# Kernel optimization log

Hardware: AMD Instinct MI355X
Metric: run time of the kernel (lower is better)

The kernel has to match this reference:

```python
import jax, jax.numpy as jnp
import numpy as np

N = 10000      # nodes
E = 160000     # edges
IN = 512       # in_feat
H = 512        # hidden_dim
L = 6          # layers
C = 64         # num_class
EPS = 1e-5     # BatchNorm eps


def setup_inputs() -> dict:
    key = jax.random.key(0)
    ks = jax.random.split(key, 12)
    x = jax.random.normal(ks[0], (N, IN), jnp.float32)
    src = jax.random.randint(ks[1], (E,), 0, N)
    dst = jax.random.randint(ks[2], (E,), 0, N)
    W0 = jax.random.normal(ks[3], (IN, H), jnp.float32) * (1.0 / np.sqrt(IN))
    Ws = jax.random.normal(ks[4], (L - 1, H, H), jnp.float32) * (1.0 / np.sqrt(H))
    bs = jnp.zeros((L, H), jnp.float32)
    gamma = jnp.ones((L, H), jnp.float32) + 0.1 * jax.random.normal(ks[5], (L, H), jnp.float32)
    beta = 0.1 * jax.random.normal(ks[6], (L, H), jnp.float32)
    run_mean = 0.1 * jax.random.normal(ks[7], (L, H), jnp.float32)
    run_var = jax.random.uniform(ks[8], (L, H), jnp.float32, 0.5, 1.5)
    linW = jax.random.normal(ks[9], (L * H, C), jnp.float32) * (1.0 / np.sqrt(L * H))
    linb = jnp.zeros((C,), jnp.float32)
    return {"x": x, "W0": W0, "Ws": Ws, "bs": bs, "gamma": gamma, "beta": beta,
            "run_mean": run_mean, "run_var": run_var, "linW": linW, "linb": linb,
            "src": src, "dst": dst}


def reference(x, W0, Ws, bs, gamma, beta, run_mean, run_var, linW, linb, src, dst):
    ones_e = jnp.ones((E,), jnp.float32)
    out_deg = jax.ops.segment_sum(ones_e, src, num_segments=N)
    in_deg = jax.ops.segment_sum(ones_e, dst, num_segments=N)
    # DGL GraphConv norm='both': D_dst^{-1/2} A D_src^{-1/2}, zero-deg clamped to 1
    norm_src = jnp.clip(out_deg, 1.0, None) ** -0.5   # [N]
    norm_dst = jnp.clip(in_deg, 1.0, None) ** -0.5    # [N]

    h = x
    hs = []
    for i in range(L):
        W = W0 if i == 0 else Ws[i - 1]
        m = (h * norm_src[:, None]) @ W                 # [N, H] GEMM
        agg = jax.ops.segment_sum(m[src], dst, num_segments=N)  # gather/scatter
        h = agg * norm_dst[:, None] + bs[i]
        # BatchNorm1d (inference, running stats) + ReLU; dropout is identity in eval
        scale = gamma[i] * jax.lax.rsqrt(run_var[i] + EPS)
        h = jax.nn.relu((h - run_mean[i]) * scale + beta[i])
        hs.append(h)
    h = jnp.concatenate(hs, axis=-1)                    # [N, L*H] JK-concat
    return h @ linW + linb                              # [N, C]
```

## Files before the change

### kernel.cpp

```cpp
#include <hip/hip_runtime.h>

#define NN 10000
#define NNPAD 10112
#define NE 160000
#define HF 512
#define LL 6
#define NC 64
#define KCAT (LL*HF)
#define BN_EPS 1e-5f
#define FSPLIT 3
#define AGG_SLOTS (((NN + 31) / 32) * 8)

typedef _Float16 f16x8 __attribute__((ext_vector_type(8)));
typedef _Float16 f16x4 __attribute__((ext_vector_type(4)));
typedef float f32x4 __attribute__((ext_vector_type(4)));

#define GLB(p) ((const __attribute__((address_space(1))) void*)(p))
#define LDSP(p) ((__attribute__((address_space(3))) void*)(p))

__global__ void deg_kernel(const int* __restrict__ src, const int* __restrict__ dst,
                           unsigned* __restrict__ cnt_out, unsigned* __restrict__ cnt_in) {
  int e = blockIdx.x * blockDim.x + threadIdx.x;
  if (e < NE) {
    atomicAdd(&cnt_out[src[e]], 1u);
    atomicAdd(&cnt_in[dst[e]], 1u);
  }
}

__global__ void fused_setup(const float* __restrict__ W0, const float* __restrict__ Ws,
                            const float* __restrict__ linW, const float* __restrict__ x,
                            const unsigned* __restrict__ cnt_out, const unsigned* __restrict__ cnt_in,
                            const float* __restrict__ bs, const float* __restrict__ gamma,
                            const float* __restrict__ beta, const float* __restrict__ rmean,
                            const float* __restrict__ rvar,
                            _Float16* __restrict__ Wt, _Float16* __restrict__ Lt,
                            _Float16* __restrict__ zh,
                            float* __restrict__ norm_src, float* __restrict__ norm_dst,
                            float* __restrict__ bnsc, float* __restrict__ bnsh) {
  __shared__ float t32[32][33];
  int b = blockIdx.x;
  int tid = threadIdx.x;
  if (b < 1536) {
    int l = b >> 8, r = b & 255;
    int n0 = (r & 15) * 32, k0 = (r >> 4) * 32;
    const float* W = (l == 0) ? W0 : (Ws + (size_t)(l - 1) * HF * HF);
    int tx = tid & 31, ty4 = (tid >> 5) * 4;
    #pragma unroll
    for (int j = 0; j < 4; ++j)
      t32[ty4 + j][tx] = W[(size_t)(k0 + ty4 + j) * HF + n0 + tx];
    __syncthreads();
    size_t base = (size_t)l * HF * HF;
    #pragma unroll
    for (int j = 0; j < 4; ++j)
      Wt[base + (size_t)(n0 + ty4 + j) * HF + k0 + tx] = (_Float16)t32[tx][ty4 + j];
  } else if (b < 1728) {
    int r = b - 1536;
    int n0 = (r & 1) * 32, k0 = (r >> 1) * 32;
    int tx = tid & 31, ty4 = (tid >> 5) * 4;
    #pragma unroll
    for (int j = 0; j < 4; ++j)
      t32[ty4 + j][tx] = linW[(size_t)(k0 + ty4 + j) * NC + n0 + tx];
    __syncthreads();
    #pragma unroll
    for (int j = 0; j < 4; ++j)
      Lt[(size_t)(n0 + ty4 + j) * KCAT + k0 + tx] = (_Float16)t32[tx][ty4 + j];
  } else if (b < 6728) {
    int i = (b - 1728) * 256 + tid;
    if (i < NN * HF / 4) {
      float4 v = *(const float4*)&x[i * 4];
      f16x4 h;
      h.x = (_Float16)v.x; h.y = (_Float16)v.y; h.z = (_Float16)v.z; h.w = (_Float16)v.w;
      *(f16x4*)&zh[i * 4] = h;
    }
  } else {
    int i = (b - 6728) * 256 + tid;
    if (i < NN) {
      unsigned co = cnt_out[i]; if (co < 1u) co = 1u;
      unsigned ci = cnt_in[i];  if (ci < 1u) ci = 1u;
      norm_src[i] = rsqrtf((float)co);
      norm_dst[i] = rsqrtf((float)ci);
    }
    if (i < LL * HF) {
      float s = gamma[i] * rsqrtf(rvar[i] + BN_EPS);
      bnsc[i] = s;
      bnsh[i] = (bs[i] - rmean[i]) * s + beta[i];
    }
  }
}

__global__ void scan_kernel(const unsigned* __restrict__ cnt, unsigned* __restrict__ off) {
  __shared__ unsigned wsum[4];
  const int T = 40;
  int tid = threadIdx.x;
  int lane = tid & 63, wv = tid >> 6;
  int start = tid * T;
  unsigned s = 0;
  for (int j = 0; j < T; ++j) {
    int i = start + j;
    if (i < NN) s += cnt[i];
  }
  unsigned x = s;
  #pragma unroll
  for (int d = 1; d < 64; d <<= 1) {
    unsigned y = __shfl_up(x, d, 64);
    if (lane >= d) x += y;
  }
  if (lane == 63) wsum[wv] = x;
  __syncthreads();
  if (tid == 0) {
    unsigned acc = 0;
    #pragma unroll
    for (int j = 0; j < 4; ++j) { acc += wsum[j]; wsum[j] = acc; }
  }
  __syncthreads();
  unsigned run = (wv ? wsum[wv - 1] : 0u) + x - s;
  for (int j = 0; j < T; ++j) {
    int i = start + j;
    if (i < NN) { off[i] = run; run += cnt[i]; }
  }
  if (tid == 0) off[NN] = wsum[3];
}

__global__ void fill_kernel(const int* __restrict__ src, const int* __restrict__ dst,
                            const unsigned* __restrict__ off, unsigned* __restrict__ cursor,
                            int* __restrict__ edge_src) {
  int e = blockIdx.x * blockDim.x + threadIdx.x;
  if (e < NE) {
    int d = dst[e];
    unsigned p = atomicAdd(&cursor[d], 1u);
    edge_src[off[d] + p] = src[e];
  }
}

__launch_bounds__(256, 2)
__global__ void gemm_layer_f16(const _Float16* __restrict__ Z, int lda,
                               const _Float16* __restrict__ Wt,
                               const float* __restrict__ nsrc,
                               _Float16* __restrict__ Mout) {
  __shared__ _Float16 As[128][64];
  __shared__ _Float16 Bs[128][64];
  int m0 = blockIdx.y * 128;
  int n0 = blockIdx.x * 128;
  int wid = threadIdx.x >> 6, lane = threadIdx.x & 63;
  int wr = wid >> 1, wc = wid & 1;
  int fr = lane & 15, kg = lane >> 4;
  int rr = lane >> 3;
  int ck = (lane & 7) ^ rr;

  f32x4 acc[4][4];
  #pragma unroll
  for (int m = 0; m < 4; ++m)
    #pragma unroll
    for (int n = 0; n < 4; ++n)
      acc[m][n] = (f32x4){0.f, 0.f, 0.f, 0.f};

  const _Float16* gA = Z  + (size_t)(m0 + wid * 32 + rr) * lda + ck * 8;
  const _Float16* gB = Wt + (size_t)(n0 + wid * 32 + rr) * HF + ck * 8;

  for (int k0 = 0; k0 < HF; k0 += 64) {
    __syncthreads();
    #pragma unroll
    for (int i = 0; i < 4; ++i) {
      __builtin_amdgcn_global_load_lds(GLB(gA + (size_t)i * 8 * lda + k0),
                                       LDSP(&As[wid * 32 + i * 8][0]), 16, 0, 0);
      __builtin_amdgcn_global_load_lds(GLB(gB + (size_t)i * 8 * HF + k0),
                                       LDSP(&Bs[wid * 32 + i * 8][0]), 16, 0, 0);
    }
    __syncthreads();
    #pragma unroll
    for (int kk = 0; kk < 2; ++kk) {
      f16x8 a[4], b[4];
      #pragma unroll
      for (int n = 0; n < 4; ++n) {
        int row = wc * 64 + n * 16 + fr;
        b[n] = *(const f16x8*)&Bs[row][((kk * 4 + kg) ^ (row & 7)) * 8];
      }
      #pragma unroll
      for (int m = 0; m < 4; ++m) {
        int row = wr * 64 + m * 16 + fr;
        a[m] = *(const f16x8*)&As[row][((kk * 4 + kg) ^ (row & 7)) * 8];
      }
      #pragma unroll
      for (int m = 0; m < 4; ++m)
        #pragma unroll
        for (int n = 0; n < 4; ++n)
          acc[m][n] = __builtin_amdgcn_mfma_f32_16x16x32_f16(a[m], b[n], acc[m][n], 0, 0, 0);
    }
  }
  #pragma unroll
  for (int m = 0; m < 4; ++m) {
    #pragma unroll
    for (int j = 0; j < 4; ++j) {
      int row = m0 + wr * 64 + m * 16 + kg * 4 + j;
      if (row < NN) {
        float s = nsrc[row];
        #pragma unroll
        for (int n = 0; n < 4; ++n) {
          int col = n0 + wc * 64 + n * 16 + fr;
          Mout[(size_t)row * HF + col] = (_Float16)(acc[m][n][j] * s);
        }
      }
    }
  }
}

__launch_bounds__(256)
__global__ void agg_bn_kernel(const _Float16* __restrict__ Mm,
                              const int* __restrict__ edge_src,
                              const unsigned* __restrict__ row_off,
                              const float* __restrict__ norm_dst,
                              const float* __restrict__ bn_scale,
                              const float* __restrict__ bn_shift,
                              _Float16* __restrict__ hcat_col) {
  int s     = blockIdx.x & 7;
  int chunk = s >> 1;
  int grp   = blockIdx.x >> 3;
  int wave  = threadIdx.x >> 6;
  int sub   = (threadIdx.x >> 4) & 3;
  int n = grp * 32 + (s & 1) * 16 + wave * 4 + sub;
  if (n >= NN) return;
  int f = chunk * 128 + (threadIdx.x & 15) * 8;
  unsigned e0 = row_off[n], e1 = row_off[n + 1];
  float a0=0.f,a1=0.f,a2=0.f,a3=0.f,a4=0.f,a5=0.f,a6=0.f,a7=0.f;
  unsigned e = e0;
  for (; e + 4 <= e1; e += 4) {
    int s0 = edge_src[e], s1 = edge_src[e + 1], s2 = edge_src[e + 2], s3 = edge_src[e + 3];
    f16x8 v0 = *(const f16x8*)&Mm[(size_t)s0 * HF + f];
    f16x8 v1 = *(const f16x8*)&Mm[(size_t)s1 * HF + f];
    f16x8 v2 = *(const f16x8*)&Mm[(size_t)s2 * HF + f];
    f16x8 v3 = *(const f16x8*)&Mm[(size_t)s3 * HF + f];
    a0 += (float)v0[0]+(float)v1[0]+(float)v2[0]+(float)v3[0];
    a1 += (float)v0[1]+(float)v1[1]+(float)v2[1]+(float)v3[1];
    a2 += (float)v0[2]+(float)v1[2]+(float)v2[2]+(float)v3[2];
    a3 += (float)v0[3]+(float)v1[3]+(float)v2[3]+(float)v3[3];
    a4 += (float)v0[4]+(float)v1[4]+(float)v2[4]+(float)v3[4];
    a5 += (float)v0[5]+(float)v1[5]+(float)v2[5]+(float)v3[5];
    a6 += (float)v0[6]+(float)v1[6]+(float)v2[6]+(float)v3[6];
    a7 += (float)v0[7]+(float)v1[7]+(float)v2[7]+(float)v3[7];
  }
  for (; e < e1; ++e) {
    int sx = edge_src[e];
    f16x8 v = *(const f16x8*)&Mm[(size_t)sx * HF + f];
    a0 += (float)v[0]; a1 += (float)v[1]; a2 += (float)v[2]; a3 += (float)v[3];
    a4 += (float)v[4]; a5 += (float)v[5]; a6 += (float)v[6]; a7 += (float)v[7];
  }
  float nd = norm_dst[n];
  float4 s0 = *(const float4*)&bn_scale[f];
  float4 s1 = *(const float4*)&bn_scale[f + 4];
  float4 t0 = *(const float4*)&bn_shift[f];
  float4 t1 = *(const float4*)&bn_shift[f + 4];
  float y0 = fmaxf(fmaf(a0 * nd, s0.x, t0.x), 0.f);
  float y1 = fmaxf(fmaf(a1 * nd, s0.y, t0.y), 0.f);
  float y2 = fmaxf(fmaf(a2 * nd, s0.z, t0.z), 0.f);
  float y3 = fmaxf(fmaf(a3 * nd, s0.w, t0.w), 0.f);
  float y4 = fmaxf(fmaf(a4 * nd, s1.x, t1.x), 0.f);
  float y5 = fmaxf(fmaf(a5 * nd, s1.y, t1.y), 0.f);
  float y6 = fmaxf(fmaf(a6 * nd, s1.z, t1.z), 0.f);
  float y7 = fmaxf(fmaf(a7 * nd, s1.w, t1.w), 0.f);
  f16x8 hv;
  hv[0]=(_Float16)y0; hv[1]=(_Float16)y1; hv[2]=(_Float16)y2; hv[3]=(_Float16)y3;
  hv[4]=(_Float16)y4; hv[5]=(_Float16)y5; hv[6]=(_Float16)y6; hv[7]=(_Float16)y7;
  *(f16x8*)&hcat_col[(size_t)n * KCAT + f] = hv;
}

__launch_bounds__(256, 2)
__global__ void final_gemm_f16(const _Float16* __restrict__ Hc,
                               const _Float16* __restrict__ Lt,
                               float* __restrict__ part) {
  __shared__ _Float16 As[128][64];
  __shared__ _Float16 Bs[64][64];
  int m0 = blockIdx.x * 128;
  int sp = blockIdx.y;
  int kbase = sp * (KCAT / FSPLIT);
  int wid = threadIdx.x >> 6, lane = threadIdx.x & 63;
  int fr = lane & 15, kg = lane >> 4;
  int rr = lane >> 3;
  int ck = (lane & 7) ^ rr;

  f32x4 acc[2][4];
  #pragma unroll
  for (int m = 0; m < 2; ++m)
    #pragma unroll
    for (int n = 0; n < 4; ++n)
      acc[m][n] = (f32x4){0.f, 0.f, 0.f, 0.f};

  const _Float16* gA = Hc + (size_t)(m0 + wid * 32 + rr) * KCAT + kbase + ck * 8;
  const _Float16* gB = Lt + (size_t)(wid * 16 + rr) * KCAT + kbase + ck * 8;

  for (int k0 = 0; k0 < KCAT / FSPLIT; k0 += 64) {
    __syncthreads();
    #pragma unroll
    for (int i = 0; i < 4; ++i)
      __builtin_amdgcn_global_load_lds(GLB(gA + (size_t)i * 8 * KCAT + k0),
                                       LDSP(&As[wid * 32 + i * 8][0]), 16, 0, 0);
    #pragma unroll
    for (int i = 0; i < 2; ++i)
      __builtin_amdgcn_global_load_lds(GLB(gB + (size_t)i * 8 * KCAT + k0),
                                       LDSP(&Bs[wid * 16 + i * 8][0]), 16, 0, 0);
    __syncthreads();
    #pragma unroll
    for (int kk = 0; kk < 2; ++kk) {
      f16x8 a[2], b[4];
      #pragma unroll
      for (int n = 0; n < 4; ++n) {
        int row = n * 16 + fr;
        b[n] = *(const f16x8*)&Bs[row][((kk * 4 + kg) ^ (row & 7)) * 8];
      }
      #pragma unroll
      for (int m = 0; m < 2; ++m) {
        int row = wid * 32 + m * 16 + fr;
        a[m] = *(const f16x8*)&As[row][((kk * 4 + kg) ^ (row & 7)) * 8];
      }
      #pragma unroll
      for (int m = 0; m < 2; ++m)
        #pragma unroll
        for (int n = 0; n < 4; ++n)
          acc[m][n] = __builtin_amdgcn_mfma_f32_16x16x32_f16(a[m], b[n], acc[m][n], 0, 0, 0);
    }
  }
  #pragma unroll
  for (int m = 0; m < 2; ++m) {
    #pragma unroll
    for (int j = 0; j < 4; ++j) {
      int row = m0 + wid * 32 + m * 16 + kg * 4 + j;
      if (row < NN) {
        #pragma unroll
        for (int n = 0; n < 4; ++n) {
          int col = n * 16 + fr;
          part[((size_t)sp * NN + row) * NC + col] = acc[m][n][j];
        }
      }
    }
  }
}

__launch_bounds__(256)
__global__ void final_reduce(const float* __restrict__ part,
                             const float* __restrict__ linb,
                             float* __restrict__ out) {
  int i = blockIdx.x * blockDim.x + threadIdx.x;
  if (i >= NN * NC / 4) return;
  int n  = i >> 4;
  int cq = i & 15;
  float4 s = *(const float4*)&linb[cq * 4];
  #pragma unroll
  for (int sp = 0; sp < FSPLIT; ++sp) {
    float4 v = *(const float4*)&part[((size_t)sp * NN + n) * NC + cq * 4];
    s.x += v.x; s.y += v.y; s.z += v.z; s.w += v.w;
  }
  *(float4*)&out[(size_t)n * NC + cq * 4] = s;
}


extern "C" void kernel_launch(void* const* d_in, const int* in_sizes, int n_in,
                              void* d_out, int out_size, void* d_ws, size_t ws_size,
                              hipStream_t stream) {
  const float* x     = (const float*)d_in[0];
  const float* W0    = (const float*)d_in[1];
  const float* Ws    = (const float*)d_in[2];
  const float* bs    = (const float*)d_in[3];
  const float* gamma = (const float*)d_in[4];
  const float* beta  = (const float*)d_in[5];
  const float* rmean = (const float*)d_in[6];
  const float* rvar  = (const float*)d_in[7];
  const float* linW  = (const float*)d_in[8];
  const float* linb  = (const float*)d_in[9];
  const int*   src   = (const int*)d_in[10];
  const int*   dst   = (const int*)d_in[11];
  float* out = (float*)d_out;

  char* w = (char*)d_ws;
  size_t o = 0;
  auto carve = [&](size_t bytes) -> void* {
    o = (o + 255) & ~(size_t)255;
    void* p = w + o;
    o += bytes;
    return p;
  };
  _Float16*  m_buf = (_Float16*)carve((size_t)NNPAD * HF * 2);
  _Float16*  hcat  = (_Float16*)carve((size_t)NNPAD * KCAT * 2);
  _Float16*  zh    = (_Float16*)carve((size_t)NNPAD * HF * 2);
  _Float16*  wt    = (_Float16*)carve((size_t)LL * HF * HF * 2);
  _Float16*  lt    = (_Float16*)carve((size_t)NC * KCAT * 2);
  float*     part  = (float*)carve((size_t)FSPLIT * NN * NC * 4);
  float*     bnsc  = (float*)carve((size_t)LL * HF * 4);
  float*     bnsh  = (float*)carve((size_t)LL * HF * 4);
  float*     nsrc  = (float*)carve((size_t)NN * 4);
  float*     ndst  = (float*)carve((size_t)NN * 4);
  unsigned*  cnts  = (unsigned*)carve((size_t)3 * NN * 4);
  unsigned*  roff  = (unsigned*)carve((size_t)(NN + 1) * 4);
  int*       esrc  = (int*)carve((size_t)NE * 4);

  unsigned* cnt_out = cnts;
  unsigned* cnt_in  = cnts + NN;
  unsigned* cursor  = cnts + 2 * NN;

  hipMemsetAsync(cnts, 0, (size_t)3 * NN * 4, stream);
  deg_kernel<<<(NE + 255) / 256, 256, 0, stream>>>(src, dst, cnt_out, cnt_in);
  fused_setup<<<6768, 256, 0, stream>>>(W0, Ws, linW, x, cnt_out, cnt_in,
                                        bs, gamma, beta, rmean, rvar,
                                        wt, lt, zh, nsrc, ndst, bnsc, bnsh);
  scan_kernel<<<1, 256, 0, stream>>>(cnt_in, roff);
  fill_kernel<<<(NE + 255) / 256, 256, 0, stream>>>(src, dst, roff, cursor, esrc);

  for (int l = 0; l < LL; ++l) {
    const _Float16* A   = (l == 0) ? zh : (hcat + (size_t)(l - 1) * HF);
    int             lda = (l == 0) ? HF : KCAT;
    gemm_layer_f16<<<dim3(HF / 128, NNPAD / 128), 256, 0, stream>>>(
        A, lda, wt + (size_t)l * HF * HF, nsrc, m_buf);
    agg_bn_kernel<<<AGG_SLOTS, 256, 0, stream>>>(m_buf, esrc, roff, ndst,
                                                 bnsc + l * HF, bnsh + l * HF,
                                                 hcat + (size_t)l * HF);
  }
  final_gemm_f16<<<dim3(NNPAD / 128, FSPLIT), 256, 0, stream>>>(hcat, lt, part);
  final_reduce<<<(NN * NC / 4 + 255) / 256, 256, 0, stream>>>(part, linb, out);
}
```

Before: 281.9 us.

## Sort aggregation rows by in-degree and fold scan into setup kernel

Builds a histogram of destination in-degrees and a counting-sort permutation of nodes, and the aggregation kernel now processes nodes in degree-sorted order. This balances the edge loop across lanes within a wave and across blocks, reducing divergence from neighbouring nodes with very different degrees. It also folds the prefix-scan kernel into the setup kernel and the permutation build into the fill kernel to remove one launch. The cost is an extra indirection per node and scattered hcat writes, since output rows are no longer contiguous per block.

```diff
diff --git a/kernel.cpp b/kernel.cpp
--- a/kernel.cpp
+++ b/kernel.cpp
@@ -36,8 +36,10 @@
                             _Float16* __restrict__ Wt, _Float16* __restrict__ Lt,
                             _Float16* __restrict__ zh,
                             float* __restrict__ norm_src, float* __restrict__ norm_dst,
-                            float* __restrict__ bnsc, float* __restrict__ bnsh) {
+                            float* __restrict__ bnsc, float* __restrict__ bnsh,
+                            unsigned* __restrict__ roff, unsigned* __restrict__ hist) {
   __shared__ float t32[32][33];
+  __shared__ unsigned wsum[4];
   int b = blockIdx.x;
   int tid = threadIdx.x;
   if (b < 1536) {
@@ -72,7 +74,7 @@
       h.x = (_Float16)v.x; h.y = (_Float16)v.y; h.z = (_Float16)v.z; h.w = (_Float16)v.w;
       *(f16x4*)&zh[i * 4] = h;
     }
-  } else {
+  } else if (b < 6768) {
     int i = (b - 6728) * 256 + tid;
     if (i < NN) {
       unsigned co = cnt_out[i]; if (co < 1u) co = 1u;
@@ -85,50 +87,71 @@
       bnsc[i] = s;
       bnsh[i] = (bs[i] - rmean[i]) * s + beta[i];
     }
-  }
-}
-
-__global__ void scan_kernel(const unsigned* __restrict__ cnt, unsigned* __restrict__ off) {
-  __shared__ unsigned wsum[4];
-  const int T = 40;
-  int tid = threadIdx.x;
-  int lane = tid & 63, wv = tid >> 6;
-  int start = tid * T;
-  unsigned s = 0;
-  for (int j = 0; j < T; ++j) {
-    int i = start + j;
-    if (i < NN) s += cnt[i];
-  }
-  unsigned x = s;
-  #pragma unroll
-  for (int d = 1; d < 64; d <<= 1) {
-    unsigned y = __shfl_up(x, d, 64);
-    if (lane >= d) x += y;
-  }
-  if (lane == 63) wsum[wv] = x;
-  __syncthreads();
-  if (tid == 0) {
-    unsigned acc = 0;
-    #pragma unroll
-    for (int j = 0; j < 4; ++j) { acc += wsum[j]; wsum[j] = acc; }
-  }
-  __syncthreads();
-  unsigned run = (wv ? wsum[wv - 1] : 0u) + x - s;
-  for (int j = 0; j < T; ++j) {
-    int i = start + j;
-    if (i < NN) { off[i] = run; run += cnt[i]; }
-  }
-  if (tid == 0) off[NN] = wsum[3];
+  } else if (b == 6768) {
+    const int T = 40;
+    int lane = tid & 63, wv = tid >> 6;
+    int start = tid * T;
+    unsigned s = 0;
+    for (int j = 0; j < T; ++j) {
+      int i = start + j;
+      if (i < NN) s += cnt_in[i];
+    }
+    unsigned xs = s;
+    #pragma unroll
+    for (int d = 1; d < 64; d <<= 1) {
+      unsigned y = __shfl_up(xs, d, 64);
+      if (lane >= d) xs += y;
+    }
+    if (lane == 63) wsum[wv] = xs;
+    __syncthreads();
+    if (tid == 0) {
+      unsigned acc = 0;
+      #pragma unroll
+      for (int j = 0; j < 4; ++j) { acc += wsum[j]; wsum[j] = acc; }
+    }
+    __syncthreads();
+    unsigned run = (wv ? wsum[wv - 1] : 0u) + xs - s;
+    for (int j = 0; j < T; ++j) {
+      int i = start + j;
+      if (i < NN) { roff[i] = run; run += cnt_in[i]; }
+    }
+    if (tid == 0) roff[NN] = wsum[3];
+  } else {
+    for (int i = tid; i < NN; i += 256) {
+      unsigned d = cnt_in[i]; if (d > 255u) d = 255u;
+      atomicAdd(&hist[d], 1u);
+    }
+  }
 }
 
 __global__ void fill_kernel(const int* __restrict__ src, const int* __restrict__ dst,
                             const unsigned* __restrict__ off, unsigned* __restrict__ cursor,
-                            int* __restrict__ edge_src) {
-  int e = blockIdx.x * blockDim.x + threadIdx.x;
-  if (e < NE) {
-    int d = dst[e];
-    unsigned p = atomicAdd(&cursor[d], 1u);
-    edge_src[off[d] + p] = src[e];
+                            int* __restrict__ edge_src,
+                            const unsigned* __restrict__ cnt_in,
+                            const unsigned* __restrict__ hist,
+                            unsigned* __restrict__ scursor,
+                            int* __restrict__ perm) {
+  int b = blockIdx.x;
+  int tid = threadIdx.x;
+  if (b < 625) {
+    int e = b * 256 + tid;
+    if (e < NE) {
+      int d = dst[e];
+      unsigned p = atomicAdd(&cursor[d], 1u);
+      edge_src[off[d] + p] = src[e];
+    }
+  } else {
+    __shared__ unsigned base_s[256];
+    if (tid == 0) {
+      unsigned acc = 0;
+      for (int j = 0; j < 256; ++j) { base_s[j] = acc; acc += hist[j]; }
+    }
+    __syncthreads();
+    for (int i = tid; i < NN; i += 256) {
+      unsigned d = cnt_in[i]; if (d > 255u) d = 255u;
+      unsigned pos = base_s[d] + atomicAdd(&scursor[d], 1u);
+      perm[pos] = i;
+    }
   }
 }
 
@@ -211,14 +234,16 @@
                               const float* __restrict__ norm_dst,
                               const float* __restrict__ bn_scale,
                               const float* __restrict__ bn_shift,
+                              const int* __restrict__ perm,
                               _Float16* __restrict__ hcat_col) {
   int s     = blockIdx.x & 7;
   int chunk = s >> 1;
   int grp   = blockIdx.x >> 3;
   int wave  = threadIdx.x >> 6;
   int sub   = (threadIdx.x >> 4) & 3;
-  int n = grp * 32 + (s & 1) * 16 + wave * 4 + sub;
-  if (n >= NN) return;
+  int ns = grp * 32 + (s & 1) * 16 + wave * 4 + sub;
+  if (ns >= NN) return;
+  int n = perm[ns];
   int f = chunk * 128 + (threadIdx.x & 15) * 8;
   unsigned e0 = row_off[n], e1 = row_off[n + 1];
   float a0=0.f,a1=0.f,a2=0.f,a3=0.f,a4=0.f,a5=0.f,a6=0.f,a7=0.f;
@@ -387,21 +412,24 @@
   float*     bnsh  = (float*)carve((size_t)LL * HF * 4);
   float*     nsrc  = (float*)carve((size_t)NN * 4);
   float*     ndst  = (float*)carve((size_t)NN * 4);
-  unsigned*  cnts  = (unsigned*)carve((size_t)3 * NN * 4);
+  unsigned*  cnts  = (unsigned*)carve(((size_t)3 * NN + 512) * 4);
   unsigned*  roff  = (unsigned*)carve((size_t)(NN + 1) * 4);
   int*       esrc  = (int*)carve((size_t)NE * 4);
+  int*       perm  = (int*)carve((size_t)NN * 4);
 
   unsigned* cnt_out = cnts;
   unsigned* cnt_in  = cnts + NN;
   unsigned* cursor  = cnts + 2 * NN;
-
-  hipMemsetAsync(cnts, 0, (size_t)3 * NN * 4, stream);
+  unsigned* hist    = cnts + 3 * NN;
+  unsigned* scursor = cnts + 3 * NN + 256;
+
+  hipMemsetAsync(cnts, 0, ((size_t)3 * NN + 512) * 4, stream);
   deg_kernel<<<(NE + 255) / 256, 256, 0, stream>>>(src, dst, cnt_out, cnt_in);
-  fused_setup<<<6768, 256, 0, stream>>>(W0, Ws, linW, x, cnt_out, cnt_in,
+  fused_setup<<<6770, 256, 0, stream>>>(W0, Ws, linW, x, cnt_out, cnt_in,
                                         bs, gamma, beta, rmean, rvar,
-                                        wt, lt, zh, nsrc, ndst, bnsc, bnsh);
-  scan_kernel<<<1, 256, 0, stream>>>(cnt_in, roff);
-  fill_kernel<<<(NE + 255) / 256, 256, 0, stream>>>(src, dst, roff, cursor, esrc);
+                                        wt, lt, zh, nsrc, ndst, bnsc, bnsh, roff, hist);
+  fill_kernel<<<626, 256, 0, stream>>>(src, dst, roff, cursor, esrc,
+                                       cnt_in, hist, scursor, perm);
 
   for (int l = 0; l < LL; ++l) {
     const _Float16* A   = (l == 0) ? zh : (hcat + (size_t)(l - 1) * HF);
@@ -410,7 +438,7 @@
         A, lda, wt + (size_t)l * HF * HF, nsrc, m_buf);
     agg_bn_kernel<<<AGG_SLOTS, 256, 0, stream>>>(m_buf, esrc, roff, ndst,
                                                  bnsc + l * HF, bnsh + l * HF,
-                                                 hcat + (size_t)l * HF);
+                                                 perm, hcat + (size_t)l * HF);
   }
   final_gemm_f16<<<dim3(NNPAD / 128, FSPLIT), 256, 0, stream>>>(hcat, lt, part);
   final_reduce<<<(NN * NC / 4 + 255) / 256, 256, 0, stream>>>(part, linb, out);
```

Result: slower. 314.3 us (+11.5%).
